# Performance work log

Hardware: AMD Instinct MI355X
Metric: run time of the kernel (lower is better)

The kernel has to match this reference:

```python
import jax, jax.numpy as jnp
import numpy as np

B, S, D = 4, 2048, 1024
H, DK, DV, DOUT = 16, 64, 64, 1024
NEG = -1.0e9


def setup_inputs() -> dict:
    key = jax.random.key(0)
    ks = jax.random.split(key, 12)
    sq = lambda fan_in: 1.0 / np.sqrt(fan_in)
    return {
        "query": jax.random.normal(ks[0], (B, S, D), jnp.float32),
        "key": jax.random.normal(ks[1], (B, S, D), jnp.float32),
        "value": jax.random.normal(ks[2], (B, S, D), jnp.float32),
        "attention_mask": jax.random.randint(ks[3], (B, 1, 1, S), 0, 2, jnp.int32),
        "wq": jax.random.normal(ks[4], (D, H * DK), jnp.float32) * sq(D),
        "bq": jnp.zeros((H * DK,), jnp.float32),
        "wk": jax.random.normal(ks[5], (D, H * DK), jnp.float32) * sq(D),
        "bk": jnp.zeros((H * DK,), jnp.float32),
        "wv": jax.random.normal(ks[6], (D, H * DV), jnp.float32) * sq(D),
        "bv": jnp.zeros((H * DV,), jnp.float32),
        "wo": jax.random.normal(ks[7], (H * DV, DOUT), jnp.float32) * sq(H * DV),
        "bo": jnp.zeros((DOUT,), jnp.float32),
    }


def _split_heads(x, head_dim):
    b, s, _ = x.shape
    return x.reshape(b, s, H, head_dim).transpose(0, 2, 1, 3)  # [B,H,S,hd]


def reference(query, key, value, attention_mask, wq, bq, wk, bk, wv, bv, wo, bo):
    q = _split_heads(query @ wq + bq, DK)   # [B,H,S,DK]
    k = _split_heads(key @ wk + bk, DK)     # [B,H,S,DK]
    v = _split_heads(value @ wv + bv, DV)   # [B,H,S,DV]
    logits = jnp.einsum("bhqd,bhkd->bhqk", q, k) / jnp.sqrt(jnp.float32(DK))
    logits = logits + attention_mask.astype(logits.dtype) * NEG
    attn = jax.nn.softmax(logits, axis=-1)
    out = jnp.einsum("bhqk,bhkd->bhqd", attn, v)          # [B,H,S,DV]
    out = out.transpose(0, 2, 1, 3).reshape(query.shape[0], -1, H * DV)
    return out @ wo + bo
```

## Files before the change

kernel.cpp:

```cpp
#include <hip/hip_runtime.h>
#include <hip/hip_bf16.h>
#include <math.h>

#define Bv 4
#define Sv 2048
#define Dv 1024
#define Hv 16
#define HD 64
#define NEGV (-1.0e9f)

typedef __attribute__((ext_vector_type(8))) short bf16x8;
typedef __attribute__((ext_vector_type(4))) short s16x4;
typedef __attribute__((ext_vector_type(4))) float f32x4;

__device__ __forceinline__ short f2bf(float f) {
    union { __hip_bfloat16 h; short s; } u;
    u.h = __float2bfloat16(f);
    return u.s;
}

__device__ __forceinline__ void glds16(const void* g, void* l) {
    __builtin_amdgcn_global_load_lds(
        (const __attribute__((address_space(1))) void*)g,
        (__attribute__((address_space(3))) void*)l, 16, 0, 0);
}

__global__ __launch_bounds__(256) void transpose_w(const float* __restrict__ W,
                                                   unsigned short* __restrict__ WT) {
    __shared__ float T[64][65];
    const int t = threadIdx.x;
    const int n0 = blockIdx.x * 64, k0 = blockIdx.y * 64;
    #pragma unroll
    for (int i = 0; i < 4; ++i) {
        const int k = (t >> 4) + 16 * i;
        const int nc = (t & 15) * 4;
        const float4 v = *(const float4*)&W[(size_t)(k0 + k) * 1024 + n0 + nc];
        T[k][nc + 0] = v.x; T[k][nc + 1] = v.y;
        T[k][nc + 2] = v.z; T[k][nc + 3] = v.w;
    }
    __syncthreads();
    const int n = t >> 2, kc = (t & 3) * 16;
    #pragma unroll
    for (int j4 = 0; j4 < 4; ++j4) {
        s16x4 o;
        #pragma unroll
        for (int jj = 0; jj < 4; ++jj) o[jj] = f2bf(T[kc + j4 * 4 + jj][n]);
        *(s16x4*)&WT[(size_t)(n0 + n) * 1024 + k0 + kc + j4 * 4] = o;
    }
}

__global__ __launch_bounds__(256) void transpose_v(const unsigned short* __restrict__ Vin,
                                                   unsigned short* __restrict__ VT) {
    __shared__ unsigned short T[64][72];
    const int t = threadIdx.x;
    const int s0 = blockIdx.x * 64;
    const int bh = blockIdx.y;
    const size_t ib = (size_t)bh * Sv * 64;
    const size_t ob = (size_t)bh * 64 * Sv;
    {
        const int s = t >> 2, dc = (t & 3) * 16;
        const bf16x8 a = *(const bf16x8*)&Vin[ib + (size_t)(s0 + s) * 64 + dc];
        const bf16x8 b = *(const bf16x8*)&Vin[ib + (size_t)(s0 + s) * 64 + dc + 8];
        *(bf16x8*)&T[s][dc] = a;
        *(bf16x8*)&T[s][dc + 8] = b;
    }
    __syncthreads();
    const int dv = t >> 2, sc = (t & 3) * 16;
    #pragma unroll
    for (int j4 = 0; j4 < 4; ++j4) {
        s16x4 o;
        #pragma unroll
        for (int jj = 0; jj < 4; ++jj) o[jj] = (short)T[sc + j4 * 4 + jj][dv];
        *(s16x4*)&VT[ob + (size_t)dv * Sv + s0 + sc + j4 * 4] = o;
    }
}

template <int PERM, bool XBF16>
__global__ __launch_bounds__(256) void gemm_mfma(const void* __restrict__ Xv,
                                                 const unsigned short* __restrict__ WT,
                                                 const float* __restrict__ bias,
                                                 void* __restrict__ Cv,
                                                 int M, int N, int K) {
    constexpr int AST = XBF16 ? 32 : 40;
    __shared__ short As[128 * AST];
    __shared__ short Bs[128 * 32];

    const int t = threadIdx.x;
    const int lane = t & 63, w = t >> 6;
    const int l15 = lane & 15, quad = lane >> 4;
    const int m0 = blockIdx.y * 128, n0 = blockIdx.x * 128;
    const int wm = (w >> 1) * 64, wn = (w & 1) * 64;

    f32x4 acc[4][4];
    #pragma unroll
    for (int mi = 0; mi < 4; ++mi)
        #pragma unroll
        for (int ni = 0; ni < 4; ++ni) acc[mi][ni] = (f32x4){0.f, 0.f, 0.f, 0.f};

    for (int k0 = 0; k0 < K; k0 += 32) {
        #pragma unroll
        for (int i = 0; i < 2; ++i) {
            const int seg = w * 2 + i;
            const int row = seg * 16 + (lane >> 2);
            const int kc = (lane & 3) * 8;
            glds16(&WT[(size_t)(n0 + row) * K + k0 + kc], &Bs[seg * 512]);
        }
        if constexpr (XBF16) {
            const unsigned short* X = (const unsigned short*)Xv;
            #pragma unroll
            for (int i = 0; i < 2; ++i) {
                const int seg = w * 2 + i;
                const int row = seg * 16 + (lane >> 2);
                const int kc = (lane & 3) * 8;
                glds16(&X[(size_t)(m0 + row) * K + k0 + kc], &As[seg * 512]);
            }
        } else {
            const float* X = (const float*)Xv;
            #pragma unroll
            for (int i = 0; i < 4; ++i) {
                const int c = t + 256 * i;
                const int row = c >> 3, kc = (c & 7) * 4;
                const float4 v = *(const float4*)&X[(size_t)(m0 + row) * K + k0 + kc];
                s16x4 bvec = {f2bf(v.x), f2bf(v.y), f2bf(v.z), f2bf(v.w)};
                *(s16x4*)&As[row * AST + kc] = bvec;
            }
        }
        __syncthreads();

        bf16x8 afr[4], bfr[4];
        #pragma unroll
        for (int mi = 0; mi < 4; ++mi)
            afr[mi] = *(const bf16x8*)&As[(wm + mi * 16 + l15) * AST + quad * 8];
        #pragma unroll
        for (int ni = 0; ni < 4; ++ni)
            bfr[ni] = *(const bf16x8*)&Bs[(wn + ni * 16 + l15) * 32 + quad * 8];
        #pragma unroll
        for (int mi = 0; mi < 4; ++mi)
            #pragma unroll
            for (int ni = 0; ni < 4; ++ni)
                acc[mi][ni] = __builtin_amdgcn_mfma_f32_16x16x32_bf16(
                    afr[mi], bfr[ni], acc[mi][ni], 0, 0, 0);
        __syncthreads();
    }

    #pragma unroll
    for (int mi = 0; mi < 4; ++mi) {
        #pragma unroll
        for (int ni = 0; ni < 4; ++ni) {
            const int col = n0 + wn + ni * 16 + l15;
            const float bsv = bias[col];
            #pragma unroll
            for (int r = 0; r < 4; ++r) {
                const int row = m0 + wm + mi * 16 + quad * 4 + r;
                const float vv = acc[mi][ni][r] + bsv;
                if constexpr (PERM == 0) {
                    ((float*)Cv)[(size_t)row * N + col] = vv;
                } else {
                    const int bb = row / Sv, s = row % Sv;
                    const int hh = col >> 6, d = col & 63;
                    ((unsigned short*)Cv)[((((size_t)bb * Hv + hh) * Sv + s) << 6) + d] =
                        (unsigned short)f2bf(vv);
                }
            }
        }
    }
}

__global__ __launch_bounds__(256) void attn_mfma(const unsigned short* __restrict__ Q,
                                                 const unsigned short* __restrict__ Kg,
                                                 const unsigned short* __restrict__ VT,
                                                 const int* __restrict__ mask,
                                                 unsigned short* __restrict__ O) {
    __shared__ short Kl[64 * 72];
    __shared__ short Vl[64 * 72];
    __shared__ short Sl[64 * 72];
    __shared__ float Mk[64];

    const int t = threadIdx.x;
    const int lane = t & 63, w = t >> 6;
    const int l15 = lane & 15, quad = lane >> 4;
    const int q0 = blockIdx.x * 64;
    const int h = blockIdx.y, b = blockIdx.z;
    const int bh = b * Hv + h;
    const size_t kvb = (size_t)bh * Sv * 64;
    const size_t vtb = (size_t)bh * 64 * Sv;

    bf16x8 qf[2];
    {
        const size_t qa = kvb + (size_t)(q0 + w * 16 + l15) * 64 + quad * 8;
        qf[0] = *(const bf16x8*)&Q[qa];
        qf[1] = *(const bf16x8*)&Q[qa + 32];
    }

    float l_acc = 0.0f;
    f32x4 oacc[4];
    #pragma unroll
    for (int ni = 0; ni < 4; ++ni) oacc[ni] = (f32x4){0.f, 0.f, 0.f, 0.f};

    const int srow = t >> 2, sch = (t & 3) * 16;

    for (int k0 = 0; k0 < Sv; k0 += 64) {
        __syncthreads();
        {
            const unsigned short* Ks = Kg + kvb + (size_t)k0 * 64;
            const bf16x8 a = *(const bf16x8*)&Ks[(size_t)srow * 64 + sch];
            const bf16x8 c = *(const bf16x8*)&Ks[(size_t)srow * 64 + sch + 8];
            *(bf16x8*)&Kl[srow * 72 + sch] = a;
            *(bf16x8*)&Kl[srow * 72 + sch + 8] = c;
            const unsigned short* Vs = VT + vtb + k0;
            const bf16x8 d = *(const bf16x8*)&Vs[(size_t)srow * Sv + sch];
            const bf16x8 e = *(const bf16x8*)&Vs[(size_t)srow * Sv + sch + 8];
            *(bf16x8*)&Vl[srow * 72 + sch] = d;
            *(bf16x8*)&Vl[srow * 72 + sch + 8] = e;
        }
        if (t < 64) Mk[t] = NEGV * (float)mask[(size_t)b * Sv + k0 + t];
        __syncthreads();

        #pragma unroll
        for (int mi = 0; mi < 4; ++mi) {
            const bf16x8 kf0 = *(const bf16x8*)&Kl[(mi * 16 + l15) * 72 + quad * 8];
            const bf16x8 kf1 = *(const bf16x8*)&Kl[(mi * 16 + l15) * 72 + 32 + quad * 8];
            f32x4 st = (f32x4){0.f, 0.f, 0.f, 0.f};
            st = __builtin_amdgcn_mfma_f32_16x16x32_bf16(kf0, qf[0], st, 0, 0, 0);
            st = __builtin_amdgcn_mfma_f32_16x16x32_bf16(kf1, qf[1], st, 0, 0, 0);
            const float4 mk4 = *(const float4*)&Mk[mi * 16 + quad * 4];
            float p0 = __expf(st[0] * 0.125f + mk4.x);
            float p1 = __expf(st[1] * 0.125f + mk4.y);
            float p2 = __expf(st[2] * 0.125f + mk4.z);
            float p3 = __expf(st[3] * 0.125f + mk4.w);
            l_acc += (p0 + p1) + (p2 + p3);
            s16x4 pv = {f2bf(p0), f2bf(p1), f2bf(p2), f2bf(p3)};
            *(s16x4*)&Sl[(w * 16 + l15) * 72 + mi * 16 + quad * 4] = pv;
        }

        const bf16x8 pf0 = *(const bf16x8*)&Sl[(w * 16 + l15) * 72 + quad * 8];
        const bf16x8 pf1 = *(const bf16x8*)&Sl[(w * 16 + l15) * 72 + 32 + quad * 8];
        #pragma unroll
        for (int ni = 0; ni < 4; ++ni) {
            const bf16x8 vf0 = *(const bf16x8*)&Vl[(ni * 16 + l15) * 72 + quad * 8];
            const bf16x8 vf1 = *(const bf16x8*)&Vl[(ni * 16 + l15) * 72 + 32 + quad * 8];
            oacc[ni] = __builtin_amdgcn_mfma_f32_16x16x32_bf16(pf0, vf0, oacc[ni], 0, 0, 0);
            oacc[ni] = __builtin_amdgcn_mfma_f32_16x16x32_bf16(pf1, vf1, oacc[ni], 0, 0, 0);
        }
    }

    l_acc += __shfl_xor(l_acc, 16);
    l_acc += __shfl_xor(l_acc, 32);
    #pragma unroll
    for (int r = 0; r < 4; ++r) {
        const float lr = __shfl(l_acc, quad * 4 + r, 64);
        const float inv = 1.0f / lr;
        const size_t row = (size_t)b * Sv + q0 + w * 16 + quad * 4 + r;
        #pragma unroll
        for (int ni = 0; ni < 4; ++ni) {
            O[row * (Hv * HD) + h * HD + ni * 16 + l15] =
                (unsigned short)f2bf(oacc[ni][r] * inv);
        }
    }
}

extern "C" void kernel_launch(void* const* d_in, const int* in_sizes, int n_in,
                              void* d_out, int out_size, void* d_ws, size_t ws_size,
                              hipStream_t stream) {
    const float* query = (const float*)d_in[0];
    const float* key   = (const float*)d_in[1];
    const float* value = (const float*)d_in[2];
    const int*   amask = (const int*)d_in[3];
    const float* wq = (const float*)d_in[4];
    const float* bq = (const float*)d_in[5];
    const float* wk = (const float*)d_in[6];
    const float* bk = (const float*)d_in[7];
    const float* wv = (const float*)d_in[8];
    const float* bv = (const float*)d_in[9];
    const float* wo = (const float*)d_in[10];
    const float* bo = (const float*)d_in[11];
    float* out = (float*)d_out;

    const size_t PBQ = (size_t)Bv * Hv * Sv * HD;
    unsigned short* wsp = (unsigned short*)d_ws;
    unsigned short* qb = wsp;
    unsigned short* kb = qb + PBQ;
    unsigned short* vb = kb + PBQ;
    unsigned short* ab = vb + PBQ;
    unsigned short* wt_ab = ab;
    unsigned short* wt_vb = vb;

    const int M = Bv * Sv;
    dim3 gt(16, 16), gg(8, M / 128), bb(256);

    transpose_w<<<gt, bb, 0, stream>>>(wv, wt_ab);
    gemm_mfma<1, false><<<gg, bb, 0, stream>>>(value, wt_ab, bv, kb, M, 1024, 1024);
    transpose_v<<<dim3(Sv / 64, Bv * Hv), bb, 0, stream>>>(kb, vb);

    transpose_w<<<gt, bb, 0, stream>>>(wq, wt_ab);
    gemm_mfma<1, false><<<gg, bb, 0, stream>>>(query, wt_ab, bq, qb, M, 1024, 1024);
    transpose_w<<<gt, bb, 0, stream>>>(wk, wt_ab);
    gemm_mfma<1, false><<<gg, bb, 0, stream>>>(key, wt_ab, bk, kb, M, 1024, 1024);

    attn_mfma<<<dim3(Sv / 64, Hv, Bv), bb, 0, stream>>>(qb, kb, vb, amask, ab);

    transpose_w<<<gt, bb, 0, stream>>>(wo, wt_vb);
    gemm_mfma<0, true><<<gg, bb, 0, stream>>>(ab, wt_vb, bo, out, M, 1024, 1024);
}
```

Before: 456.4 us.

## Pre-convert inputs to bf16, double query tile per attention block, add per-batch fallback

A separate conversion kernel casts the fp32 activations to bf16, so every GEMM can load both operands through global_load_lds instead of converting in registers. The attention kernel now handles 128 query rows per block (32 per wave), so each K/V tile staged in LDS serves twice as many queries. A new fallback path processes one batch at a time when the workspace is small. The price is three extra conversion launches with their memory traffic, plus more registers and LDS per attention block, which halves the attention grid.

```diff
diff --git a/kernel.cpp b/kernel.cpp
--- a/kernel.cpp
+++ b/kernel.cpp
@@ -23,6 +23,16 @@
     __builtin_amdgcn_global_load_lds(
         (const __attribute__((address_space(1))) void*)g,
         (__attribute__((address_space(3))) void*)l, 16, 0, 0);
+}
+
+__global__ __launch_bounds__(256) void cvt_bf16(const float* __restrict__ X,
+                                                unsigned short* __restrict__ Y) {
+    const size_t i = ((size_t)blockIdx.x * 256 + threadIdx.x) * 8;
+    const float4 a = *(const float4*)&X[i];
+    const float4 b = *(const float4*)&X[i + 4];
+    bf16x8 o = {f2bf(a.x), f2bf(a.y), f2bf(a.z), f2bf(a.w),
+                f2bf(b.x), f2bf(b.y), f2bf(b.z), f2bf(b.w)};
+    *(bf16x8*)&Y[i] = o;
 }
 
 __global__ __launch_bounds__(256) void transpose_w(const float* __restrict__ W,
@@ -75,14 +85,13 @@
     }
 }
 
-template <int PERM, bool XBF16>
-__global__ __launch_bounds__(256) void gemm_mfma(const void* __restrict__ Xv,
+template <int PERM>
+__global__ __launch_bounds__(256) void gemm_mfma(const unsigned short* __restrict__ X,
                                                  const unsigned short* __restrict__ WT,
                                                  const float* __restrict__ bias,
                                                  void* __restrict__ Cv,
                                                  int M, int N, int K) {
-    constexpr int AST = XBF16 ? 32 : 40;
-    __shared__ short As[128 * AST];
+    __shared__ short As[128 * 32];
     __shared__ short Bs[128 * 32];
 
     const int t = threadIdx.x;
@@ -97,40 +106,23 @@
         #pragma unroll
         for (int ni = 0; ni < 4; ++ni) acc[mi][ni] = (f32x4){0.f, 0.f, 0.f, 0.f};
 
+    const int srow = lane >> 2;
+    const int skc = (lane & 3) * 8;
+
     for (int k0 = 0; k0 < K; k0 += 32) {
         #pragma unroll
         for (int i = 0; i < 2; ++i) {
             const int seg = w * 2 + i;
-            const int row = seg * 16 + (lane >> 2);
-            const int kc = (lane & 3) * 8;
-            glds16(&WT[(size_t)(n0 + row) * K + k0 + kc], &Bs[seg * 512]);
-        }
-        if constexpr (XBF16) {
-            const unsigned short* X = (const unsigned short*)Xv;
-            #pragma unroll
-            for (int i = 0; i < 2; ++i) {
-                const int seg = w * 2 + i;
-                const int row = seg * 16 + (lane >> 2);
-                const int kc = (lane & 3) * 8;
-                glds16(&X[(size_t)(m0 + row) * K + k0 + kc], &As[seg * 512]);
-            }
-        } else {
-            const float* X = (const float*)Xv;
-            #pragma unroll
-            for (int i = 0; i < 4; ++i) {
-                const int c = t + 256 * i;
-                const int row = c >> 3, kc = (c & 7) * 4;
-                const float4 v = *(const float4*)&X[(size_t)(m0 + row) * K + k0 + kc];
-                s16x4 bvec = {f2bf(v.x), f2bf(v.y), f2bf(v.z), f2bf(v.w)};
-                *(s16x4*)&As[row * AST + kc] = bvec;
-            }
+            const int row = seg * 16 + srow;
+            glds16(&WT[(size_t)(n0 + row) * K + k0 + skc], &Bs[seg * 512]);
+            glds16(&X[(size_t)(m0 + row) * K + k0 + skc], &As[seg * 512]);
         }
         __syncthreads();
 
         bf16x8 afr[4], bfr[4];
         #pragma unroll
         for (int mi = 0; mi < 4; ++mi)
-            afr[mi] = *(const bf16x8*)&As[(wm + mi * 16 + l15) * AST + quad * 8];
+            afr[mi] = *(const bf16x8*)&As[(wm + mi * 16 + l15) * 32 + quad * 8];
         #pragma unroll
         for (int ni = 0; ni < 4; ++ni)
             bfr[ni] = *(const bf16x8*)&Bs[(wn + ni * 16 + l15) * 32 + quad * 8];
@@ -173,29 +165,32 @@
                                                  unsigned short* __restrict__ O) {
     __shared__ short Kl[64 * 72];
     __shared__ short Vl[64 * 72];
-    __shared__ short Sl[64 * 72];
+    __shared__ short Sl[128 * 72];
     __shared__ float Mk[64];
 
     const int t = threadIdx.x;
     const int lane = t & 63, w = t >> 6;
     const int l15 = lane & 15, quad = lane >> 4;
-    const int q0 = blockIdx.x * 64;
+    const int q0 = blockIdx.x * 128;
     const int h = blockIdx.y, b = blockIdx.z;
     const int bh = b * Hv + h;
     const size_t kvb = (size_t)bh * Sv * 64;
     const size_t vtb = (size_t)bh * 64 * Sv;
 
-    bf16x8 qf[2];
-    {
-        const size_t qa = kvb + (size_t)(q0 + w * 16 + l15) * 64 + quad * 8;
-        qf[0] = *(const bf16x8*)&Q[qa];
-        qf[1] = *(const bf16x8*)&Q[qa + 32];
-    }
-
-    float l_acc = 0.0f;
-    f32x4 oacc[4];
-    #pragma unroll
-    for (int ni = 0; ni < 4; ++ni) oacc[ni] = (f32x4){0.f, 0.f, 0.f, 0.f};
+    bf16x8 qf[2][2];
+    #pragma unroll
+    for (int ni = 0; ni < 2; ++ni) {
+        const size_t qa = kvb + (size_t)(q0 + w * 32 + ni * 16 + l15) * 64 + quad * 8;
+        qf[ni][0] = *(const bf16x8*)&Q[qa];
+        qf[ni][1] = *(const bf16x8*)&Q[qa + 32];
+    }
+
+    float l_acc[2] = {0.f, 0.f};
+    f32x4 oacc[2][4];
+    #pragma unroll
+    for (int mi = 0; mi < 2; ++mi)
+        #pragma unroll
+        for (int ni = 0; ni < 4; ++ni) oacc[mi][ni] = (f32x4){0.f, 0.f, 0.f, 0.f};
 
     const int srow = t >> 2, sch = (t & 3) * 16;
 
@@ -220,41 +215,51 @@
         for (int mi = 0; mi < 4; ++mi) {
             const bf16x8 kf0 = *(const bf16x8*)&Kl[(mi * 16 + l15) * 72 + quad * 8];
             const bf16x8 kf1 = *(const bf16x8*)&Kl[(mi * 16 + l15) * 72 + 32 + quad * 8];
-            f32x4 st = (f32x4){0.f, 0.f, 0.f, 0.f};
-            st = __builtin_amdgcn_mfma_f32_16x16x32_bf16(kf0, qf[0], st, 0, 0, 0);
-            st = __builtin_amdgcn_mfma_f32_16x16x32_bf16(kf1, qf[1], st, 0, 0, 0);
             const float4 mk4 = *(const float4*)&Mk[mi * 16 + quad * 4];
-            float p0 = __expf(st[0] * 0.125f + mk4.x);
-            float p1 = __expf(st[1] * 0.125f + mk4.y);
-            float p2 = __expf(st[2] * 0.125f + mk4.z);
-            float p3 = __expf(st[3] * 0.125f + mk4.w);
-            l_acc += (p0 + p1) + (p2 + p3);
-            s16x4 pv = {f2bf(p0), f2bf(p1), f2bf(p2), f2bf(p3)};
-            *(s16x4*)&Sl[(w * 16 + l15) * 72 + mi * 16 + quad * 4] = pv;
-        }
-
-        const bf16x8 pf0 = *(const bf16x8*)&Sl[(w * 16 + l15) * 72 + quad * 8];
-        const bf16x8 pf1 = *(const bf16x8*)&Sl[(w * 16 + l15) * 72 + 32 + quad * 8];
-        #pragma unroll
-        for (int ni = 0; ni < 4; ++ni) {
-            const bf16x8 vf0 = *(const bf16x8*)&Vl[(ni * 16 + l15) * 72 + quad * 8];
-            const bf16x8 vf1 = *(const bf16x8*)&Vl[(ni * 16 + l15) * 72 + 32 + quad * 8];
-            oacc[ni] = __builtin_amdgcn_mfma_f32_16x16x32_bf16(pf0, vf0, oacc[ni], 0, 0, 0);
-            oacc[ni] = __builtin_amdgcn_mfma_f32_16x16x32_bf16(pf1, vf1, oacc[ni], 0, 0, 0);
-        }
-    }
-
-    l_acc += __shfl_xor(l_acc, 16);
-    l_acc += __shfl_xor(l_acc, 32);
-    #pragma unroll
-    for (int r = 0; r < 4; ++r) {
-        const float lr = __shfl(l_acc, quad * 4 + r, 64);
-        const float inv = 1.0f / lr;
-        const size_t row = (size_t)b * Sv + q0 + w * 16 + quad * 4 + r;
-        #pragma unroll
-        for (int ni = 0; ni < 4; ++ni) {
-            O[row * (Hv * HD) + h * HD + ni * 16 + l15] =
-                (unsigned short)f2bf(oacc[ni][r] * inv);
+            #pragma unroll
+            for (int ni = 0; ni < 2; ++ni) {
+                f32x4 st = (f32x4){0.f, 0.f, 0.f, 0.f};
+                st = __builtin_amdgcn_mfma_f32_16x16x32_bf16(kf0, qf[ni][0], st, 0, 0, 0);
+                st = __builtin_amdgcn_mfma_f32_16x16x32_bf16(kf1, qf[ni][1], st, 0, 0, 0);
+                const float p0 = __expf(st[0] * 0.125f + mk4.x);
+                const float p1 = __expf(st[1] * 0.125f + mk4.y);
+                const float p2 = __expf(st[2] * 0.125f + mk4.z);
+                const float p3 = __expf(st[3] * 0.125f + mk4.w);
+                l_acc[ni] += (p0 + p1) + (p2 + p3);
+                s16x4 pv = {f2bf(p0), f2bf(p1), f2bf(p2), f2bf(p3)};
+                *(s16x4*)&Sl[(w * 32 + ni * 16 + l15) * 72 + mi * 16 + quad * 4] = pv;
+            }
+        }
+
+        #pragma unroll
+        for (int mi = 0; mi < 2; ++mi) {
+            const bf16x8 pf0 = *(const bf16x8*)&Sl[(w * 32 + mi * 16 + l15) * 72 + quad * 8];
+            const bf16x8 pf1 = *(const bf16x8*)&Sl[(w * 32 + mi * 16 + l15) * 72 + 32 + quad * 8];
+            #pragma unroll
+            for (int ni = 0; ni < 4; ++ni) {
+                const bf16x8 vf0 = *(const bf16x8*)&Vl[(ni * 16 + l15) * 72 + quad * 8];
+                const bf16x8 vf1 = *(const bf16x8*)&Vl[(ni * 16 + l15) * 72 + 32 + quad * 8];
+                oacc[mi][ni] = __builtin_amdgcn_mfma_f32_16x16x32_bf16(pf0, vf0, oacc[mi][ni], 0, 0, 0);
+                oacc[mi][ni] = __builtin_amdgcn_mfma_f32_16x16x32_bf16(pf1, vf1, oacc[mi][ni], 0, 0, 0);
+            }
+        }
+    }
+
+    #pragma unroll
+    for (int mi = 0; mi < 2; ++mi) {
+        float l = l_acc[mi];
+        l += __shfl_xor(l, 16);
+        l += __shfl_xor(l, 32);
+        #pragma unroll
+        for (int r = 0; r < 4; ++r) {
+            const float lr = __shfl(l, quad * 4 + r, 64);
+            const float inv = 1.0f / lr;
+            const size_t row = (size_t)b * Sv + q0 + w * 32 + mi * 16 + quad * 4 + r;
+            #pragma unroll
+            for (int ni = 0; ni < 4; ++ni) {
+                O[row * (Hv * HD) + h * HD + ni * 16 + l15] =
+                    (unsigned short)f2bf(oacc[mi][ni][r] * inv);
+            }
         }
     }
 }
@@ -276,29 +281,71 @@
     const float* bo = (const float*)d_in[11];
     float* out = (float*)d_out;
 
-    const size_t PBQ = (size_t)Bv * Hv * Sv * HD;
     unsigned short* wsp = (unsigned short*)d_ws;
-    unsigned short* qb = wsp;
-    unsigned short* kb = qb + PBQ;
-    unsigned short* vb = kb + PBQ;
-    unsigned short* ab = vb + PBQ;
-    unsigned short* wt_ab = ab;
-    unsigned short* wt_vb = vb;
-
-    const int M = Bv * Sv;
-    dim3 gt(16, 16), gg(8, M / 128), bb(256);
-
-    transpose_w<<<gt, bb, 0, stream>>>(wv, wt_ab);
-    gemm_mfma<1, false><<<gg, bb, 0, stream>>>(value, wt_ab, bv, kb, M, 1024, 1024);
-    transpose_v<<<dim3(Sv / 64, Bv * Hv), bb, 0, stream>>>(kb, vb);
-
-    transpose_w<<<gt, bb, 0, stream>>>(wq, wt_ab);
-    gemm_mfma<1, false><<<gg, bb, 0, stream>>>(query, wt_ab, bq, qb, M, 1024, 1024);
-    transpose_w<<<gt, bb, 0, stream>>>(wk, wt_ab);
-    gemm_mfma<1, false><<<gg, bb, 0, stream>>>(key, wt_ab, bk, kb, M, 1024, 1024);
-
-    attn_mfma<<<dim3(Sv / 64, Hv, Bv), bb, 0, stream>>>(qb, kb, vb, amask, ab);
-
-    transpose_w<<<gt, bb, 0, stream>>>(wo, wt_vb);
-    gemm_mfma<0, true><<<gg, bb, 0, stream>>>(ab, wt_vb, bo, out, M, 1024, 1024);
-}
+    dim3 bb(256), gt(16, 16);
+
+    if (ws_size >= (size_t)64 * 1024 * 1024) {
+        const size_t PBQ = (size_t)Bv * Hv * Sv * HD;
+        unsigned short* qb = wsp;
+        unsigned short* kb = qb + PBQ;
+        unsigned short* vb = kb + PBQ;
+        unsigned short* ab = vb + PBQ;
+        unsigned short* wt_kb = kb;
+        unsigned short* wt_out = (unsigned short*)d_out;
+        unsigned short* wt_vb = vb;
+
+        const int M = Bv * Sv;
+        dim3 gg(8, M / 128), gc(M * 1024 / 2048);
+
+        cvt_bf16<<<gc, bb, 0, stream>>>(value, ab);
+        transpose_w<<<gt, bb, 0, stream>>>(wv, wt_kb);
+        gemm_mfma<1><<<gg, bb, 0, stream>>>(ab, wt_kb, bv, qb, M, 1024, 1024);
+        transpose_v<<<dim3(Sv / 64, Bv * Hv), bb, 0, stream>>>(qb, vb);
+
+        cvt_bf16<<<gc, bb, 0, stream>>>(query, ab);
+        transpose_w<<<gt, bb, 0, stream>>>(wq, wt_kb);
+        gemm_mfma<1><<<gg, bb, 0, stream>>>(ab, wt_kb, bq, qb, M, 1024, 1024);
+
+        cvt_bf16<<<gc, bb, 0, stream>>>(key, ab);
+        transpose_w<<<gt, bb, 0, stream>>>(wk, wt_out);
+        gemm_mfma<1><<<gg, bb, 0, stream>>>(ab, wt_out, bk, kb, M, 1024, 1024);
+
+        attn_mfma<<<dim3(Sv / 128, Hv, Bv), bb, 0, stream>>>(qb, kb, vb, amask, ab);
+
+        transpose_w<<<gt, bb, 0, stream>>>(wo, wt_vb);
+        gemm_mfma<0><<<gg, bb, 0, stream>>>(ab, wt_vb, bo, out, M, 1024, 1024);
+    } else {
+        const size_t PQ = (size_t)Hv * Sv * HD;
+        unsigned short* qb = wsp;
+        unsigned short* kb = qb + PQ;
+        unsigned short* vb = kb + PQ;
+        unsigned short* ab = vb + PQ;
+        const int M = Sv;
+        dim3 gg(8, M / 128), gc(M * 1024 / 2048);
+        for (int b = 0; b < Bv; ++b) {
+            const size_t xoff = (size_t)b * Sv * Dv;
+            unsigned short* wt_kb = kb;
+            unsigned short* wt_out = (unsigned short*)(out + xoff);
+            unsigned short* wt_vb = vb;
+
+            cvt_bf16<<<gc, bb, 0, stream>>>(value + xoff, ab);
+            transpose_w<<<gt, bb, 0, stream>>>(wv, wt_kb);
+            gemm_mfma<1><<<gg, bb, 0, stream>>>(ab, wt_kb, bv, qb, M, 1024, 1024);
+            transpose_v<<<dim3(Sv / 64, Hv), bb, 0, stream>>>(qb, vb);
+
+            cvt_bf16<<<gc, bb, 0, stream>>>(query + xoff, ab);
+            transpose_w<<<gt, bb, 0, stream>>>(wq, wt_kb);
+            gemm_mfma<1><<<gg, bb, 0, stream>>>(ab, wt_kb, bq, qb, M, 1024, 1024);
+
+            cvt_bf16<<<gc, bb, 0, stream>>>(key + xoff, ab);
+            transpose_w<<<gt, bb, 0, stream>>>(wk, wt_out);
+            gemm_mfma<1><<<gg, bb, 0, stream>>>(ab, wt_out, bk, kb, M, 1024, 1024);
+
+            attn_mfma<<<dim3(Sv / 128, Hv, 1), bb, 0, stream>>>(qb, kb, vb,
+                                                                amask + (size_t)b * Sv, ab);
+
+            transpose_w<<<gt, bb, 0, stream>>>(wo, wt_vb);
+            gemm_mfma<0><<<gg, bb, 0, stream>>>(ab, wt_vb, bo, out + xoff, M, 1024, 1024);
+        }
+    }
+}
```

Result: faster. 409.3 us (-10.3%).
